# Kernel tuning notes

Hardware: AMD Instinct MI355X
Metric: run time of the kernel (lower is better)

Reference implementation:

```python
import jax, jax.numpy as jnp
import numpy as np

MARGIN = 1.0

def _safe_sqrt(x):
    # sqrt with zero gradient at x<=0 (matches relu().sqrt() forward; avoids NaN grads on the zero diagonal)
    pos = x > 0
    return jnp.where(pos, jnp.sqrt(jnp.where(pos, x, 1.0)), 0.0)

def _smoothed_metric_loss(X, m=MARGIN):
    # X: [N, d], N even; lifted-structure smoothed loss (Song et al.)
    N = X.shape[0]
    sq = jnp.sum(X * X, axis=1)                       # [N]
    G = X @ X.T                                       # [N, N]
    D = _safe_sqrt(jax.nn.relu(sq[:, None] + sq[None, :] - 2.0 * G))
    E = jnp.exp(m - D)                                # [N, N]
    P = N // 2
    i = jnp.arange(P) * 2
    j = i + 1
    # negatives for pair p: rows {i,j}, all cols except {i,j}
    row_pair_sum = E.reshape(P, 2, N).sum(axis=(1, 2))  # [P] = rowsum(i)+rowsum(j)
    excl = E[i, i] + E[i, j] + E[j, i] + E[j, j]
    neg_sum = row_pair_sum - excl
    J = jnp.log(neg_sum) + D[i, j]
    return jnp.sum(jax.nn.relu(J) ** 2) / (2.0 * P)

def reference(text_embeddings, shape_embeddings):
    N = text_embeddings.shape[0]
    # tt loss on text embeddings
    metric_tt = _smoothed_metric_loss(text_embeddings, MARGIN)
    # repeat each shape embedding twice (index_select with i//2)
    shape_rep = jnp.repeat(shape_embeddings, 2, axis=0)  # [N, d]
    mask = jnp.tile(jnp.array([1.0, 0.0], dtype=text_embeddings.dtype), N // 2)[:, None]
    inv = 1.0 - mask
    e1 = text_embeddings * mask + shape_rep * inv
    e2 = text_embeddings * inv + shape_rep * mask
    emb = jnp.concatenate([e1, e2], axis=0)              # [2N, d]
    metric_st = _smoothed_metric_loss(emb, MARGIN)
    return metric_tt + metric_st

def setup_inputs() -> dict:
    key = jax.random.key(0)
    k1, k2 = jax.random.split(key)
    N, Dim = 4096, 256
    text = jax.random.normal(k1, (N, Dim), dtype=jnp.float32)
    shape = jax.random.normal(k2, (N // 2, Dim), dtype=jnp.float32)
    return {"text_embeddings": text, "shape_embeddings": shape}
```

## Files before the change

kernel.cpp:

```cpp
#include <hip/hip_runtime.h>
#include <hip/hip_bf16.h>
#include <math.h>


typedef __bf16 bf16x8 __attribute__((ext_vector_type(8)));
typedef float floatx4 __attribute__((ext_vector_type(4)));

#define KD 256
#define NU 6144
#define NBU 48
#define TU (NBU * (NBU + 1) / 2)
#define BM 128
#define BK 32
#define ECONST 2.718281828459045f
#define LOSS_BLOCKS 1536

#define LSLOT(r, q) ((((r) * 4 + ((q) ^ (((r) >> 1) & 3)))) * 8)

__device__ __forceinline__ void gload_lds16(const void* g, void* l) {
  __builtin_amdgcn_global_load_lds((const __attribute__((address_space(1))) unsigned int*)g,
                                   (__attribute__((address_space(3))) unsigned int*)l,
                                   16, 0, 0);
}

__global__ __launch_bounds__(256) void prep_kernel(const float* __restrict__ text,
                                                   const float* __restrict__ shape,
                                                   __bf16* __restrict__ Xu,
                                                   float* __restrict__ sq,
                                                   float* __restrict__ rowacc) {
  int gt = blockIdx.x * 256 + threadIdx.x;
  if (gt < 2 * NU) rowacc[gt] = 0.f;
  int wave = gt >> 6;
  int lane = gt & 63;
  const float* src = (wave < 4096) ? (text + (size_t)wave * KD)
                                   : (shape + (size_t)(wave - 4096) * KD);
  __bf16* dst = Xu + (size_t)wave * KD;
  float s = 0.f;
#pragma unroll
  for (int j = 0; j < 4; ++j) {
    int idx = j * 64 + lane;
    float f = src[idx];
    __bf16 h = (__bf16)f;
    dst[idx] = h;
    float fv = (float)h;
    s += fv * fv;
  }
#pragma unroll
  for (int m = 1; m < 64; m <<= 1) s += __shfl_xor(s, m, 64);
  if (lane == 0) sq[wave] = s;
}

__global__ __launch_bounds__(256, 4) void egemm_tri_kernel(
    const __bf16* __restrict__ X, const float* __restrict__ sq,
    float* __restrict__ rowacc) {
  __shared__ __align__(16) __bf16 As[BM * BK];
  __shared__ __align__(16) __bf16 Bs[BM * BK];
  __shared__ float rowbuf[2][128];
  __shared__ float colbuf[2][128];

  int t = blockIdx.x;
  int by = (int)((sqrtf(8.0f * (float)t + 1.0f) - 1.0f) * 0.5f);
  while ((by + 1) * (by + 2) / 2 <= t) ++by;
  while (by * (by + 1) / 2 > t) --by;
  const int bx = t - by * (by + 1) / 2;

  const int mBase = by * BM;
  const int nBase = bx * BM;
  const bool diag = (by == bx);

  const int tid = threadIdx.x;
  const int lane = tid & 63;
  const int w = tid >> 6;
  const int warpM = w >> 1, warpN = w & 1;
  const int quad = lane >> 4;
  const int l15 = lane & 15;

  floatx4 acc[4][4] = {};

  const int sRow = lane >> 2;
  const int sCol = (((lane & 3) ^ ((lane >> 3) & 3))) * 8;

  for (int kt = 0; kt < KD; kt += BK) {
    __syncthreads();
#pragma unroll
    for (int h = 0; h < 2; ++h) {
      int c = h * 4 + w;
      gload_lds16(X + (size_t)(mBase + c * 16 + sRow) * KD + kt + sCol, &As[c * 512]);
      gload_lds16(X + (size_t)(nBase + c * 16 + sRow) * KD + kt + sCol, &Bs[c * 512]);
    }
    __syncthreads();

    bf16x8 af[4], bfr[4];
#pragma unroll
    for (int tm = 0; tm < 4; ++tm)
      af[tm] = *(const bf16x8*)&As[LSLOT(warpM * 64 + tm * 16 + l15, quad)];
#pragma unroll
    for (int tn = 0; tn < 4; ++tn)
      bfr[tn] = *(const bf16x8*)&Bs[LSLOT(warpN * 64 + tn * 16 + l15, quad)];
#pragma unroll
    for (int tm = 0; tm < 4; ++tm)
#pragma unroll
      for (int tn = 0; tn < 4; ++tn)
        acc[tm][tn] = __builtin_amdgcn_mfma_f32_16x16x32_bf16(af[tm], bfr[tn], acc[tm][tn], 0, 0, 0);
  }

  const int rbase = mBase + warpM * 64;
  const int cbase = nBase + warpN * 64;
  float sqr[4][4], sqc[4];
#pragma unroll
  for (int tm = 0; tm < 4; ++tm)
#pragma unroll
    for (int r = 0; r < 4; ++r)
      sqr[tm][r] = sq[rbase + tm * 16 + quad * 4 + r];
#pragma unroll
  for (int tn = 0; tn < 4; ++tn)
    sqc[tn] = sq[cbase + tn * 16 + l15];

  const float L2E = 1.44269504088896f;
  float cs[4] = {0.f, 0.f, 0.f, 0.f};
#pragma unroll
  for (int tm = 0; tm < 4; ++tm) {
    float rs[4] = {0.f, 0.f, 0.f, 0.f};
#pragma unroll
    for (int tn = 0; tn < 4; ++tn) {
#pragma unroll
      for (int r = 0; r < 4; ++r) {
        float v = acc[tm][tn][r];
        float dsq = fmaf(-2.0f, v, sqr[tm][r] + sqc[tn]);
        float dst = sqrtf(fmaxf(dsq, 0.f));
        float ev = __builtin_amdgcn_exp2f(fmaf(-L2E, dst, L2E));
        if (diag && tm == tn && (quad * 4 + r) == l15) ev = 0.f;
        rs[r] += ev;
        cs[tn] += ev;
      }
    }
#pragma unroll
    for (int r = 0; r < 4; ++r) {
      float v = rs[r];
      v += __shfl_xor(v, 1, 64);
      v += __shfl_xor(v, 2, 64);
      v += __shfl_xor(v, 4, 64);
      v += __shfl_xor(v, 8, 64);
      if (l15 == 0) rowbuf[warpN][warpM * 64 + tm * 16 + quad * 4 + r] = v;
    }
  }
#pragma unroll
  for (int tn = 0; tn < 4; ++tn) {
    float v = cs[tn];
    v += __shfl_xor(v, 16, 64);
    v += __shfl_xor(v, 32, 64);
    if (quad == 0) colbuf[warpM][warpN * 64 + tn * 16 + l15] = v;
  }
  __syncthreads();

  float* rdst = rowacc + (bx < 32 ? 0 : NU);
  float* cdst = rowacc + (by < 32 ? 0 : NU);
  if (tid < 128) {
    atomicAdd(&rdst[mBase + tid], rowbuf[0][tid] + rowbuf[1][tid]);
  } else if (!diag) {
    int c = tid - 128;
    atomicAdd(&cdst[nBase + c], colbuf[0][c] + colbuf[1][c]);
  }
}

__global__ __launch_bounds__(256) void loss_kernel(const float* __restrict__ text,
                                                   const float* __restrict__ shape,
                                                   const float* __restrict__ rowacc,
                                                   float* __restrict__ partials) {
  __shared__ float part[4];
  const float* St = rowacc;
  const float* Ss = rowacc + NU;
  int wv = blockIdx.x * 4 + (threadIdx.x >> 6);
  int lane = threadIdx.x & 63;
  const float *a, *b;
  float base, scale;
  if (wv < 2048) {
    int p = wv;
    a = text + (size_t)(2 * p) * KD;
    b = text + (size_t)(2 * p + 1) * KD;
    base = St[2 * p] + St[2 * p + 1];
    scale = 1.0f / 4096.0f;
  } else {
    int p = wv - 2048;
    int u1, u2;
    if (p < 2048) {
      u1 = 2 * p; u2 = 4096 + p;
      a = text + (size_t)(2 * p) * KD;
      b = shape + (size_t)p * KD;
    } else {
      int s = p - 2048;
      u1 = 4096 + s; u2 = 2 * s + 1;
      a = shape + (size_t)s * KD;
      b = text + (size_t)(2 * s + 1) * KD;
    }
    float g1 = St[u1] + 2.0f * Ss[u1];
    float g2 = St[u2] + 2.0f * Ss[u2];
    base = g1 + g2 + ECONST;
    scale = 1.0f / 8192.0f;
  }
  float s = 0.f;
#pragma unroll
  for (int j = 0; j < 4; ++j) {
    int idx = j * 64 + lane;
    float d = a[idx] - b[idx];
    s += d * d;
  }
#pragma unroll
  for (int m = 1; m < 64; m <<= 1) s += __shfl_xor(s, m, 64);
  if (lane == 0) {
    float D = s > 0.f ? sqrtf(s) : 0.f;
    float ns = base - 2.0f * expf(1.0f - D);
    float J = logf(ns) + D;
    part[threadIdx.x >> 6] = (J > 0.f) ? J * J * scale : 0.f;
  }
  __syncthreads();
  if (threadIdx.x == 0)
    partials[blockIdx.x] = part[0] + part[1] + part[2] + part[3];
}

__global__ __launch_bounds__(256) void reduce_kernel(const float* __restrict__ partials,
                                                     float* __restrict__ out, int out_n) {
  __shared__ float part[4];
  float s = 0.f;
  for (int i = threadIdx.x; i < LOSS_BLOCKS; i += 256) s += partials[i];
#pragma unroll
  for (int m = 1; m < 64; m <<= 1) s += __shfl_xor(s, m, 64);
  if ((threadIdx.x & 63) == 0) part[threadIdx.x >> 6] = s;
  __syncthreads();
  if (threadIdx.x == 0) out[0] = part[0] + part[1] + part[2] + part[3];
  else if (threadIdx.x < out_n) out[threadIdx.x] = 0.f;
}

extern "C" void kernel_launch(void* const* d_in, const int* in_sizes, int n_in,
                              void* d_out, int out_size, void* d_ws, size_t ws_size,
                              hipStream_t stream) {
  const float* text = (const float*)d_in[0];
  const float* shape = (const float*)d_in[1];
  float* out = (float*)d_out;

  char* ws = (char*)d_ws;
  __bf16* Xu = (__bf16*)ws;
  float* sq = (float*)(ws + (size_t)NU * KD * 2);
  float* rowacc = sq + NU;
  float* partials = rowacc + 2 * NU;

  prep_kernel<<<NU / 4, 256, 0, stream>>>(text, shape, Xu, sq, rowacc);
  egemm_tri_kernel<<<TU, 256, 0, stream>>>(Xu, sq, rowacc);
  loss_kernel<<<LOSS_BLOCKS, 256, 0, stream>>>(text, shape, rowacc, partials);
  reduce_kernel<<<1, 256, 0, stream>>>(partials, out, out_size);
}
```

Measured before the change: 100.1 us.

## Fuse prep, triangular GEMM and loss into one cooperative persistent kernel

Replaces the four separate launches with a single cooperative kernel that does the bf16 conversion, the triangular exp-GEMM tiles in a persistent loop, and the pair loss, separated by grid-wide syncs. The final reduction becomes one atomic add per block. This is meant to remove kernel launch gaps and tail effects between stages. In exchange it adds grid sync overhead, caps occupancy at about 768 blocks with launch bounds of 3 waves per SIMD, and serialises tiles inside each block. The old multi-kernel path is kept as a fallback.

```diff
diff --git a/kernel.cpp b/kernel.cpp
--- a/kernel.cpp
+++ b/kernel.cpp
@@ -1,6 +1,9 @@
 #include <hip/hip_runtime.h>
 #include <hip/hip_bf16.h>
+#include <hip/hip_cooperative_groups.h>
 #include <math.h>
+
+namespace cg = cooperative_groups;
 
 
 typedef __bf16 bf16x8 __attribute__((ext_vector_type(8)));
@@ -13,6 +16,7 @@
 #define BM 128
 #define BK 32
 #define ECONST 2.718281828459045f
+#define NBLK 768
 #define LOSS_BLOCKS 1536
 
 #define LSLOT(r, q) ((((r) * 4 + ((q) ^ (((r) >> 1) & 3)))) * 8)
@@ -21,6 +25,203 @@
   __builtin_amdgcn_global_load_lds((const __attribute__((address_space(1))) unsigned int*)g,
                                    (__attribute__((address_space(3))) unsigned int*)l,
                                    16, 0, 0);
+}
+
+__global__ __launch_bounds__(256, 3) void fused_kernel(
+    const float* __restrict__ text, const float* __restrict__ shape,
+    __bf16* __restrict__ Xu, float* __restrict__ sq,
+    float* __restrict__ rowacc,
+    float* __restrict__ out, int out_n) {
+  __shared__ __align__(16) __bf16 As[BM * BK];
+  __shared__ __align__(16) __bf16 Bs[BM * BK];
+  __shared__ float rowbuf[2][128];
+  __shared__ float colbuf[2][128];
+  __shared__ float part[4];
+
+  const int tid = threadIdx.x;
+  const int lane = tid & 63;
+  const int w = tid >> 6;
+  const int bid = blockIdx.x;
+  const int nblk = gridDim.x;
+  const int gt = bid * 256 + tid;
+
+  for (int i = gt; i < 2 * NU; i += nblk * 256) rowacc[i] = 0.f;
+  if (gt < out_n) out[gt] = 0.f;
+  for (int wave = bid * 4 + w; wave < NU; wave += nblk * 4) {
+    const float* src = (wave < 4096) ? (text + (size_t)wave * KD)
+                                     : (shape + (size_t)(wave - 4096) * KD);
+    __bf16* dst = Xu + (size_t)wave * KD;
+    float s = 0.f;
+#pragma unroll
+    for (int j = 0; j < 4; ++j) {
+      int idx = j * 64 + lane;
+      float f = src[idx];
+      __bf16 h = (__bf16)f;
+      dst[idx] = h;
+      float fv = (float)h;
+      s += fv * fv;
+    }
+#pragma unroll
+    for (int m = 1; m < 64; m <<= 1) s += __shfl_xor(s, m, 64);
+    if (lane == 0) sq[wave] = s;
+  }
+  __threadfence();
+  cg::this_grid().sync();
+  __threadfence();
+
+  const int warpM = w >> 1, warpN = w & 1;
+  const int quad = lane >> 4;
+  const int l15 = lane & 15;
+  const int sRow = lane >> 2;
+  const int sCol = (((lane & 3) ^ ((lane >> 3) & 3))) * 8;
+  const float L2E = 1.44269504088896f;
+
+  for (int t = bid; t < TU; t += nblk) {
+    int by = (int)((sqrtf(8.0f * (float)t + 1.0f) - 1.0f) * 0.5f);
+    while ((by + 1) * (by + 2) / 2 <= t) ++by;
+    while (by * (by + 1) / 2 > t) --by;
+    const int bx = t - by * (by + 1) / 2;
+
+    const int mBase = by * BM;
+    const int nBase = bx * BM;
+    const bool diag = (by == bx);
+
+    floatx4 acc[4][4] = {};
+
+    for (int kt = 0; kt < KD; kt += BK) {
+      __syncthreads();
+#pragma unroll
+      for (int h = 0; h < 2; ++h) {
+        int c = h * 4 + w;
+        gload_lds16(Xu + (size_t)(mBase + c * 16 + sRow) * KD + kt + sCol, &As[c * 512]);
+        gload_lds16(Xu + (size_t)(nBase + c * 16 + sRow) * KD + kt + sCol, &Bs[c * 512]);
+      }
+      __syncthreads();
+
+      bf16x8 af[4], bfr[4];
+#pragma unroll
+      for (int tm = 0; tm < 4; ++tm)
+        af[tm] = *(const bf16x8*)&As[LSLOT(warpM * 64 + tm * 16 + l15, quad)];
+#pragma unroll
+      for (int tn = 0; tn < 4; ++tn)
+        bfr[tn] = *(const bf16x8*)&Bs[LSLOT(warpN * 64 + tn * 16 + l15, quad)];
+#pragma unroll
+      for (int tm = 0; tm < 4; ++tm)
+#pragma unroll
+        for (int tn = 0; tn < 4; ++tn)
+          acc[tm][tn] = __builtin_amdgcn_mfma_f32_16x16x32_bf16(af[tm], bfr[tn], acc[tm][tn], 0, 0, 0);
+    }
+
+    const int rbase = mBase + warpM * 64;
+    const int cbase = nBase + warpN * 64;
+    float sqr[4][4], sqc[4];
+#pragma unroll
+    for (int tm = 0; tm < 4; ++tm)
+#pragma unroll
+      for (int r = 0; r < 4; ++r)
+        sqr[tm][r] = sq[rbase + tm * 16 + quad * 4 + r];
+#pragma unroll
+    for (int tn = 0; tn < 4; ++tn)
+      sqc[tn] = sq[cbase + tn * 16 + l15];
+
+    float cs[4] = {0.f, 0.f, 0.f, 0.f};
+#pragma unroll
+    for (int tm = 0; tm < 4; ++tm) {
+      float rs[4] = {0.f, 0.f, 0.f, 0.f};
+#pragma unroll
+      for (int tn = 0; tn < 4; ++tn) {
+#pragma unroll
+        for (int r = 0; r < 4; ++r) {
+          float v = acc[tm][tn][r];
+          float dsq = fmaf(-2.0f, v, sqr[tm][r] + sqc[tn]);
+          float dst = sqrtf(fmaxf(dsq, 0.f));
+          float ev = __builtin_amdgcn_exp2f(fmaf(-L2E, dst, L2E));
+          if (diag && tm == tn && (quad * 4 + r) == l15) ev = 0.f;
+          rs[r] += ev;
+          cs[tn] += ev;
+        }
+      }
+#pragma unroll
+      for (int r = 0; r < 4; ++r) {
+        float v = rs[r];
+        v += __shfl_xor(v, 1, 64);
+        v += __shfl_xor(v, 2, 64);
+        v += __shfl_xor(v, 4, 64);
+        v += __shfl_xor(v, 8, 64);
+        if (l15 == 0) rowbuf[warpN][warpM * 64 + tm * 16 + quad * 4 + r] = v;
+      }
+    }
+#pragma unroll
+    for (int tn = 0; tn < 4; ++tn) {
+      float v = cs[tn];
+      v += __shfl_xor(v, 16, 64);
+      v += __shfl_xor(v, 32, 64);
+      if (quad == 0) colbuf[warpM][warpN * 64 + tn * 16 + l15] = v;
+    }
+    __syncthreads();
+
+    float* rdst = rowacc + (bx < 32 ? 0 : NU);
+    float* cdst = rowacc + (by < 32 ? 0 : NU);
+    if (tid < 128) {
+      atomicAdd(&rdst[mBase + tid], rowbuf[0][tid] + rowbuf[1][tid]);
+    } else if (!diag) {
+      int c = tid - 128;
+      atomicAdd(&cdst[nBase + c], colbuf[0][c] + colbuf[1][c]);
+    }
+  }
+  __threadfence();
+  cg::this_grid().sync();
+  __threadfence();
+
+  const float* St = rowacc;
+  const float* Ss = rowacc + NU;
+  float jacc = 0.f;
+  for (int wv = bid * 4 + w; wv < NU; wv += nblk * 4) {
+    const float *a, *b;
+    float base, scale;
+    if (wv < 2048) {
+      int p = wv;
+      a = text + (size_t)(2 * p) * KD;
+      b = text + (size_t)(2 * p + 1) * KD;
+      base = St[2 * p] + St[2 * p + 1];
+      scale = 1.0f / 4096.0f;
+    } else {
+      int p = wv - 2048;
+      int u1, u2;
+      if (p < 2048) {
+        u1 = 2 * p; u2 = 4096 + p;
+        a = text + (size_t)(2 * p) * KD;
+        b = shape + (size_t)p * KD;
+      } else {
+        int s = p - 2048;
+        u1 = 4096 + s; u2 = 2 * s + 1;
+        a = shape + (size_t)s * KD;
+        b = text + (size_t)(2 * s + 1) * KD;
+      }
+      float g1 = St[u1] + 2.0f * Ss[u1];
+      float g2 = St[u2] + 2.0f * Ss[u2];
+      base = g1 + g2 + ECONST;
+      scale = 1.0f / 8192.0f;
+    }
+    float s = 0.f;
+#pragma unroll
+    for (int j = 0; j < 4; ++j) {
+      int idx = j * 64 + lane;
+      float d = a[idx] - b[idx];
+      s += d * d;
+    }
+#pragma unroll
+    for (int m = 1; m < 64; m <<= 1) s += __shfl_xor(s, m, 64);
+    if (lane == 0) {
+      float D = s > 0.f ? sqrtf(s) : 0.f;
+      float ns = base - 2.0f * expf(1.0f - D);
+      float J = logf(ns) + D;
+      jacc += (J > 0.f) ? J * J * scale : 0.f;
+    }
+  }
+  if (lane == 0) part[w] = jacc;
+  __syncthreads();
+  if (tid == 0) atomicAdd(out, part[0] + part[1] + part[2] + part[3]);
 }
 
 __global__ __launch_bounds__(256) void prep_kernel(const float* __restrict__ text,
@@ -244,8 +445,42 @@
   float* rowacc = sq + NU;
   float* partials = rowacc + 2 * NU;
 
-  prep_kernel<<<NU / 4, 256, 0, stream>>>(text, shape, Xu, sq, rowacc);
-  egemm_tri_kernel<<<TU, 256, 0, stream>>>(Xu, sq, rowacc);
-  loss_kernel<<<LOSS_BLOCKS, 256, 0, stream>>>(text, shape, rowacc, partials);
-  reduce_kernel<<<1, 256, 0, stream>>>(partials, out, out_size);
-}
+  static int coop_grid = -2;
+  if (coop_grid == -2) {
+    hipDeviceProp_t prop;
+    int maxB = 0;
+    if (hipGetDeviceProperties(&prop, 0) == hipSuccess &&
+        prop.cooperativeLaunch &&
+        hipOccupancyMaxActiveBlocksPerMultiprocessor(
+            &maxB, (const void*)fused_kernel, 256, 0) == hipSuccess &&
+        maxB > 0) {
+      long g = (long)maxB * prop.multiProcessorCount;
+      coop_grid = (int)(g > NBLK ? NBLK : g);
+    } else {
+      coop_grid = -1;
+    }
+  }
+
+  bool done = false;
+  if (coop_grid > 0) {
+    int out_n = out_size;
+    void* kargs[] = {(void*)&text, (void*)&shape, (void*)&Xu, (void*)&sq,
+                     (void*)&rowacc, (void*)&out, (void*)&out_n};
+    hipError_t e = hipLaunchCooperativeKernel((const void*)fused_kernel,
+                                              dim3(coop_grid), dim3(256), kargs,
+                                              0, stream);
+    if (e == hipSuccess) {
+      done = true;
+    } else {
+      (void)hipGetLastError();
+      coop_grid = -1;
+    }
+  }
+
+  if (!done) {
+    prep_kernel<<<NU / 4, 256, 0, stream>>>(text, shape, Xu, sq, rowacc);
+    egemm_tri_kernel<<<TU, 256, 0, stream>>>(Xu, sq, rowacc);
+    loss_kernel<<<LOSS_BLOCKS, 256, 0, stream>>>(text, shape, rowacc, partials);
+    reduce_kernel<<<1, 256, 0, stream>>>(partials, out, out_size);
+  }
+}
```

Result: slower. 242.5 us (+142.3%).
